# Optimization experiments

Measured on AMD Instinct MI355X. Metric: run time of the kernel, lower is better.

The kernel has to match this reference:

```python
import jax, jax.numpy as jnp
import numpy as np

K = 1024          # num_embeddings
D = 128           # embedding_dim
EMA_DECAY = 0.99
EPS = 1e-5


def setup_inputs() -> dict:
    key = jax.random.key(0)
    k1, k2, k3 = jax.random.split(key, 3)
    z = jax.random.normal(k1, (64, D, 32, 32), dtype=jnp.float32)
    codebook = jax.random.normal(k2, (K, D), dtype=jnp.float32)
    ema_count = jnp.zeros((K,), dtype=jnp.float32)
    ema_weight = jax.random.normal(k3, (K, D), dtype=jnp.float32)
    return {"z": z, "codebook": codebook, "ema_count": ema_count, "ema_weight": ema_weight}


def reference(z, codebook, ema_count, ema_weight):
    B, C, H, W = z.shape
    # flatten to [N, D] in BHWC order (matches permute(0,2,3,1).view(-1, D))
    z_flat = jnp.transpose(z, (0, 2, 3, 1)).reshape(-1, D)  # [N, D]

    # squared euclidean distances [N, K]
    distances = (
        jnp.sum(z_flat * z_flat, axis=1, keepdims=True)
        + jnp.sum(codebook * codebook, axis=1)
        - 2.0 * jnp.matmul(z_flat, codebook.T)
    )
    indices = jnp.argmin(distances, axis=1)  # [N] int

    # gather instead of one-hot @ codebook (same math)
    quantized_flat = codebook[indices]  # [N, D]
    # NOTE: faithful to original: raw view of BHWC-ordered flat buffer into z.shape
    quantized = quantized_flat.reshape(z.shape)

    # EMA statistics (no_grad in original): segment sums instead of one-hot matmuls
    encodings_sum = jax.ops.segment_sum(jnp.ones_like(indices, dtype=jnp.float32), indices, num_segments=K)
    dw = jax.ops.segment_sum(z_flat, indices, num_segments=K)  # [K, D]
    new_ema_count = EMA_DECAY * ema_count + (1.0 - EMA_DECAY) * encodings_sum
    new_ema_weight = EMA_DECAY * ema_weight + (1.0 - EMA_DECAY) * dw
    n = jnp.sum(new_ema_count)
    weights = (new_ema_count + EPS) / (n + K * EPS) * n
    new_codebook = new_ema_weight / weights[:, None]

    commitment_loss = jnp.mean((jax.lax.stop_gradient(quantized) - z) ** 2)
    codebook_loss = jnp.mean((quantized - jax.lax.stop_gradient(z)) ** 2)

    # straight-through estimator
    quantized_st = z + jax.lax.stop_gradient(quantized - z)

    idx_map = indices.reshape(B, H, W)
    return (quantized_st, idx_map, commitment_loss, codebook_loss,
            new_codebook, new_ema_count, new_ema_weight)
```

## Files before the change

### kernel.cpp

```cpp
#include <hip/hip_runtime.h>

#define NVEC 65536
#define KCB  1024
#define DIM  128
#define HW   1024
#define CHUNK 64
#define NCHUNKS (NVEC / CHUNK)

typedef __bf16 b16;
typedef b16 b16x8 __attribute__((ext_vector_type(8)));
typedef float f32x16 __attribute__((ext_vector_type(16)));

static __device__ __forceinline__ unsigned short f2bf(float f) {
  unsigned int x = __float_as_uint(f);
  unsigned int r = x + 0x7fffu + ((x >> 16) & 1u);
  return (unsigned short)(r >> 16);
}

__global__ void k_prep(const float* __restrict__ cb, const float* __restrict__ emw,
                       uint4* __restrict__ cbt, float* __restrict__ ccb,
                       double* __restrict__ cc64, float* __restrict__ out6,
                       int* __restrict__ hist) {
  const int t = blockIdx.x * blockDim.x + threadIdx.x;
  const int kc = t >> 11, u = t & 2047;
  const int code7 = u & 127, dch = u >> 7;
  const float* src = cb + (kc * 128 + code7) * 128 + dch * 8;
  const float4 x = *(const float4*)src;
  const float4 y = *(const float4*)(src + 4);
  uint4 o;
  o.x = (unsigned)f2bf(x.x) | ((unsigned)f2bf(x.y) << 16);
  o.y = (unsigned)f2bf(x.z) | ((unsigned)f2bf(x.w) << 16);
  o.z = (unsigned)f2bf(y.x) | ((unsigned)f2bf(y.y) << 16);
  o.w = (unsigned)f2bf(y.z) | ((unsigned)f2bf(y.w) << 16);
  cbt[t] = o;
  const float4 e0 = *(const float4*)(emw + (size_t)t * 8);
  const float4 e1 = *(const float4*)(emw + (size_t)t * 8 + 4);
  *(float2*)(out6 + (size_t)t * 8 + 0) = make_float2(0.99f * e0.x, 0.99f * e0.y);
  *(float2*)(out6 + (size_t)t * 8 + 2) = make_float2(0.99f * e0.z, 0.99f * e0.w);
  *(float2*)(out6 + (size_t)t * 8 + 4) = make_float2(0.99f * e1.x, 0.99f * e1.y);
  *(float2*)(out6 + (size_t)t * 8 + 6) = make_float2(0.99f * e1.z, 0.99f * e1.w);
  if (t < KCB) hist[t] = 0;
  if (blockIdx.x < 4) {
    const int k = blockIdx.x * 256 + threadIdx.x;
    const float* row = cb + k * DIM;
    double s = 0.0;
#pragma unroll 8
    for (int j = 0; j < DIM; ++j) {
      const double v = (double)row[j];
      s = fma(v, v, s);
    }
    cc64[k] = s;
    ccb[k] = 512.f - 0.5f * (float)s;
  }
}

__global__ __launch_bounds__(256, 4) void k_argmin3t(
    const float* __restrict__ z, const uint4* __restrict__ cbt,
    const float* __restrict__ ccb, uint2* __restrict__ pcand,
    float* __restrict__ z_t) {
  __shared__ __align__(16) char smem[128 * 65 * 4];
  float (*zs)[65] = (float(*)[65])smem;
  uint4* Bs = (uint4*)smem;
  const int tid = threadIdx.x;
  const int l = tid & 63, wv = tid >> 6;
  const int g = l >> 5;
  const int lm = l & 31;
  const int wr = (wv & 1) * 32;
  const int wc = wv >> 1;
  const int n0 = blockIdx.x * 64;
  const int b = n0 >> 10;
  const int hwbase = n0 & (HW - 1);

  {
    const int hw4 = (tid & 15) * 4;
    const int dr = tid >> 4;
    const float* src = z + (size_t)b * 131072 + hwbase + hw4;
#pragma unroll
    for (int j = 0; j < 8; ++j) {
      const int d = dr + 16 * j;
      const float4 v = *(const float4*)(src + d * 1024);
      zs[d][hw4 + 0] = v.x; zs[d][hw4 + 1] = v.y;
      zs[d][hw4 + 2] = v.z; zs[d][hw4 + 3] = v.w;
    }
  }
  __syncthreads();

#pragma unroll
  for (int jj = 0; jj < 2; ++jj) {
    const int row = (tid >> 3) + 32 * jj;
    float* dst = z_t + ((size_t)(n0 + row)) * 128;
#pragma unroll
    for (int j = 0; j < 4; ++j) {
      const int d = (j * 8 + (tid & 7)) * 4;
      float4 v;
      v.x = zs[d + 0][row]; v.y = zs[d + 1][row];
      v.z = zs[d + 2][row]; v.w = zs[d + 3][row];
      *(float4*)(dst + d) = v;
    }
  }
  uint4 afrag[8];
  {
    const int row = wr + lm;
#pragma unroll
    for (int ks = 0; ks < 8; ++ks) {
      const int d0 = ks * 16 + g * 8;
      afrag[ks].x = (unsigned)f2bf(zs[d0 + 0][row]) | ((unsigned)f2bf(zs[d0 + 1][row]) << 16);
      afrag[ks].y = (unsigned)f2bf(zs[d0 + 2][row]) | ((unsigned)f2bf(zs[d0 + 3][row]) << 16);
      afrag[ks].z = (unsigned)f2bf(zs[d0 + 4][row]) | ((unsigned)f2bf(zs[d0 + 5][row]) << 16);
      afrag[ks].w = (unsigned)f2bf(zs[d0 + 6][row]) | ((unsigned)f2bf(zs[d0 + 7][row]) << 16);
    }
  }

  unsigned pm1[16], pm2[16];
#pragma unroll
  for (int r = 0; r < 16; ++r) { pm1[r] = 0u; pm2[r] = 0u; }

  for (int kc = 0; kc < 8; ++kc) {
    __syncthreads();
#pragma unroll
    for (int i = 0; i < 8; ++i) {
      __builtin_amdgcn_global_load_lds(&cbt[kc * 2048 + wv * 512 + i * 64 + l],
                                       &Bs[wv * 512 + i * 64], 16, 0, 0);
    }
    const float cv0 = ccb[kc * 128 + (wc * 2 + 0) * 32 + lm];
    const float cv1 = ccb[kc * 128 + (wc * 2 + 1) * 32 + lm];
    __syncthreads();

    f32x16 a0, a1;
#pragma unroll
    for (int j = 0; j < 16; ++j) { a0[j] = cv0; a1[j] = cv1; }
#pragma unroll
    for (int ks = 0; ks < 8; ++ks) {
      const b16x8 av = *reinterpret_cast<const b16x8*>(&afrag[ks]);
      const b16x8 bv0 = *reinterpret_cast<const b16x8*>(&Bs[(ks * 2 + g) * 128 + (wc * 2) * 32 + lm]);
      const b16x8 bv1 = *reinterpret_cast<const b16x8*>(&Bs[(ks * 2 + g) * 128 + (wc * 2 + 1) * 32 + lm]);
      a0 = __builtin_amdgcn_mfma_f32_32x32x16_bf16(av, bv0, a0, 0, 0, 0);
      a1 = __builtin_amdgcn_mfma_f32_32x32x16_bf16(av, bv1, a1, 0, 0, 0);
    }
    const unsigned ci0 = 1023u - (unsigned)(kc * 128 + (wc * 2) * 32 + lm);
    const unsigned ci1 = ci0 - 32u;
#pragma unroll
    for (int r = 0; r < 16; ++r) {
      {
        const unsigned uu = ((__float_as_uint(a0[r]) + 0x200u) & 0xFFFFFC00u) | ci0;
        const unsigned t = pm1[r] < uu ? pm1[r] : uu;
        pm1[r] = pm1[r] > uu ? pm1[r] : uu;
        pm2[r] = pm2[r] > t ? pm2[r] : t;
      }
      {
        const unsigned uu = ((__float_as_uint(a1[r]) + 0x200u) & 0xFFFFFC00u) | ci1;
        const unsigned t = pm1[r] < uu ? pm1[r] : uu;
        pm1[r] = pm1[r] > uu ? pm1[r] : uu;
        pm2[r] = pm2[r] > t ? pm2[r] : t;
      }
    }
  }

#pragma unroll
  for (int r = 0; r < 16; ++r) {
    unsigned u1 = pm1[r], u2 = pm2[r];
#pragma unroll
    for (int m = 1; m < 32; m <<= 1) {
      const unsigned o1 = (unsigned)__shfl_xor((int)u1, m, 64);
      const unsigned o2 = (unsigned)__shfl_xor((int)u2, m, 64);
      const unsigned s = u1 < o1 ? u1 : o1;
      u1 = u1 > o1 ? u1 : o1;
      u2 = u2 > o2 ? u2 : o2;
      u2 = u2 > s ? u2 : s;
    }
    if (lm == 0) {
      const int rowg = n0 + wr + (r & 3) + 8 * (r >> 2) + 4 * g;
      pcand[wc * NVEC + rowg] = make_uint2(u1, u2);
    }
  }
}

__global__ void k_rescore_hist(const float* __restrict__ z_t, const float* __restrict__ cb,
                               const double* __restrict__ cc64,
                               const uint2* __restrict__ pcand,
                               float* __restrict__ out1, int* __restrict__ hist) {
  __shared__ int h[KCB];
  const int tid = threadIdx.x;
#pragma unroll
  for (int j = 0; j < 4; ++j) h[tid + 256 * j] = 0;
  __syncthreads();
  const int n = blockIdx.x * 256 + tid;
  const uint2 A = pcand[n];
  const uint2 Bq = pcand[NVEC + n];
  int ks[4];
  ks[0] = 1023 - (int)(A.x & 1023u);
  ks[1] = 1023 - (int)(A.y & 1023u);
  ks[2] = 1023 - (int)(Bq.x & 1023u);
  ks[3] = 1023 - (int)(Bq.y & 1023u);
  const float4* zr = (const float4*)(z_t + (size_t)n * DIM);
  const float4* c0 = (const float4*)(cb + ks[0] * DIM);
  const float4* c1 = (const float4*)(cb + ks[1] * DIM);
  const float4* c2 = (const float4*)(cb + ks[2] * DIM);
  const float4* c3 = (const float4*)(cb + ks[3] * DIM);
  double d0 = 0.0, d1 = 0.0, d2 = 0.0, d3 = 0.0;
#pragma unroll 4
  for (int j = 0; j < DIM / 4; ++j) {
    const float4 zv = zr[j];
    const double zx = zv.x, zy = zv.y, zz = zv.z, zw = zv.w;
    const float4 a = c0[j];
    d0 = fma(zx, (double)a.x, d0); d0 = fma(zy, (double)a.y, d0);
    d0 = fma(zz, (double)a.z, d0); d0 = fma(zw, (double)a.w, d0);
    const float4 b = c1[j];
    d1 = fma(zx, (double)b.x, d1); d1 = fma(zy, (double)b.y, d1);
    d1 = fma(zz, (double)b.z, d1); d1 = fma(zw, (double)b.w, d1);
    const float4 c = c2[j];
    d2 = fma(zx, (double)c.x, d2); d2 = fma(zy, (double)c.y, d2);
    d2 = fma(zz, (double)c.z, d2); d2 = fma(zw, (double)c.w, d2);
    const float4 e = c3[j];
    d3 = fma(zx, (double)e.x, d3); d3 = fma(zy, (double)e.y, d3);
    d3 = fma(zz, (double)e.z, d3); d3 = fma(zw, (double)e.w, d3);
  }
  double s[4];
  s[0] = fma(-2.0, d0, cc64[ks[0]]);
  s[1] = fma(-2.0, d1, cc64[ks[1]]);
  s[2] = fma(-2.0, d2, cc64[ks[2]]);
  s[3] = fma(-2.0, d3, cc64[ks[3]]);
  int kw = ks[0]; double sw = s[0];
#pragma unroll
  for (int c = 1; c < 4; ++c) {
    if (s[c] < sw || (s[c] == sw && ks[c] < kw)) { sw = s[c]; kw = ks[c]; }
  }
  out1[n] = (float)kw;
  atomicAdd(&h[kw], 1);
  __syncthreads();
#pragma unroll
  for (int j = 0; j < 4; ++j) {
    const int v = h[tid + 256 * j];
    if (v) atomicAdd(&hist[tid + 256 * j], v);
  }
}

__global__ void k_scan(const int* __restrict__ hist, const float* __restrict__ emc,
                       int* __restrict__ cursor, float* __restrict__ out5,
                       float* __restrict__ ntot) {
  __shared__ int tmp[KCB];
  __shared__ float red[16];
  const int t = threadIdx.x;
  const int v = hist[t];
  tmp[t] = v;
  __syncthreads();
  for (int off = 1; off < KCB; off <<= 1) {
    int x = 0;
    if (t >= off) x = tmp[t - off];
    __syncthreads();
    if (t >= off) tmp[t] += x;
    __syncthreads();
  }
  cursor[t] = tmp[t] - v;
  float o5 = 0.99f * emc[t] + 0.01f * (float)v;
  out5[t] = o5;
#pragma unroll
  for (int m = 32; m; m >>= 1) o5 += __shfl_xor(o5, m, 64);
  if ((t & 63) == 0) red[t >> 6] = o5;
  __syncthreads();
  if (t == 0) {
    float s = 0.f;
#pragma unroll
    for (int j = 0; j < 16; ++j) s += red[j];
    *ntot = s;
  }
}

__global__ void k_scatter(const float* __restrict__ idx_f, int* __restrict__ cursor,
                          int* __restrict__ order, int* __restrict__ key) {
  const int n = blockIdx.x * blockDim.x + threadIdx.x;
  const int k = (int)idx_f[n];
  const int pos = atomicAdd(&cursor[k], 1);
  order[pos] = n;
  key[pos] = k;
}

__global__ __launch_bounds__(128) void k_chunkreduce_q(
    float* zq, const float* __restrict__ cb,
    const int* __restrict__ order, const int* __restrict__ key,
    float* __restrict__ out6, float* __restrict__ lossp) {
  __shared__ int so[CHUNK], sk[CHUNK];
  __shared__ float red[2];
  const int t = threadIdx.x;
  const int base = blockIdx.x * CHUNK;
  if (t < CHUNK) { so[t] = order[base + t]; sk[t] = key[base + t]; }
  __syncthreads();
  int kprev = sk[0];
  float cbv = cb[kprev * 128 + t];
  float acc = 0.f, loss = 0.f;
  int i = 0;
  while (i < CHUNK) {
    if (i + 8 <= CHUNK && sk[i] == kprev && sk[i + 7] == kprev) {
      const int n0 = so[i + 0], n1 = so[i + 1], n2 = so[i + 2], n3 = so[i + 3];
      const int n4 = so[i + 4], n5 = so[i + 5], n6 = so[i + 6], n7 = so[i + 7];
      const float v0 = zq[(size_t)n0 * 128 + t];
      const float v1 = zq[(size_t)n1 * 128 + t];
      const float v2 = zq[(size_t)n2 * 128 + t];
      const float v3 = zq[(size_t)n3 * 128 + t];
      const float v4 = zq[(size_t)n4 * 128 + t];
      const float v5 = zq[(size_t)n5 * 128 + t];
      const float v6 = zq[(size_t)n6 * 128 + t];
      const float v7 = zq[(size_t)n7 * 128 + t];
      acc += ((v0 + v1) + (v2 + v3)) + ((v4 + v5) + (v6 + v7));
      float e;
      e = cbv - v0; loss = fmaf(e, e, loss);
      e = cbv - v1; loss = fmaf(e, e, loss);
      e = cbv - v2; loss = fmaf(e, e, loss);
      e = cbv - v3; loss = fmaf(e, e, loss);
      e = cbv - v4; loss = fmaf(e, e, loss);
      e = cbv - v5; loss = fmaf(e, e, loss);
      e = cbv - v6; loss = fmaf(e, e, loss);
      e = cbv - v7; loss = fmaf(e, e, loss);
      zq[(size_t)n0 * 128 + t] = cbv; zq[(size_t)n1 * 128 + t] = cbv;
      zq[(size_t)n2 * 128 + t] = cbv; zq[(size_t)n3 * 128 + t] = cbv;
      zq[(size_t)n4 * 128 + t] = cbv; zq[(size_t)n5 * 128 + t] = cbv;
      zq[(size_t)n6 * 128 + t] = cbv; zq[(size_t)n7 * 128 + t] = cbv;
      i += 8;
    } else {
      const int kk = sk[i];
      if (kk != kprev) {
        atomicAdd(&out6[kprev * 128 + t], 0.01f * acc);
        acc = 0.f; kprev = kk;
        cbv = cb[kk * 128 + t];
      }
      const int n = so[i];
      const float v = zq[(size_t)n * 128 + t];
      acc += v;
      const float e = cbv - v; loss = fmaf(e, e, loss);
      zq[(size_t)n * 128 + t] = cbv;
      ++i;
    }
  }
  atomicAdd(&out6[kprev * 128 + t], 0.01f * acc);
#pragma unroll
  for (int m = 32; m; m >>= 1) loss += __shfl_xor(loss, m, 64);
  if ((t & 63) == 0) red[t >> 6] = loss;
  __syncthreads();
  if (t == 0) lossp[blockIdx.x] = red[0] + red[1];
}

__global__ void k_final(const float* __restrict__ out5, const float* __restrict__ out6,
                        const float* __restrict__ ntot_p, const float* __restrict__ lossp,
                        float* __restrict__ out4, float* __restrict__ out2,
                        float* __restrict__ out3) {
  __shared__ float red[4];
  const int i = blockIdx.x * blockDim.x + threadIdx.x;
  const float ntot = *ntot_p;
  const int k = i >> 7;
  const float w = (out5[k] + 1e-5f) / (ntot + KCB * 1e-5f) * ntot;
  out4[i] = out6[i] / w;
  if (blockIdx.x == 511) {
    const int t = threadIdx.x;
    float s = 0.f;
#pragma unroll
    for (int j = 0; j < NCHUNKS / 256; ++j) s += lossp[t + 256 * j];
#pragma unroll
    for (int m = 32; m; m >>= 1) s += __shfl_xor(s, m, 64);
    if ((t & 63) == 0) red[t >> 6] = s;
    __syncthreads();
    if (t == 0) {
      const float lv = (red[0] + red[1] + red[2] + red[3]) * (1.f / 8388608.f);
      *out2 = lv; *out3 = lv;
    }
  }
}

extern "C" void kernel_launch(void* const* d_in, const int* in_sizes, int n_in,
                              void* d_out, int out_size, void* d_ws, size_t ws_size,
                              hipStream_t stream) {
  (void)in_sizes; (void)n_in; (void)out_size; (void)ws_size;
  const float* z   = (const float*)d_in[0];
  const float* cb  = (const float*)d_in[1];
  const float* emc = (const float*)d_in[2];
  const float* emw = (const float*)d_in[3];
  float* out = (float*)d_out;
  float* out0 = out;
  float* out1 = out + 8388608;
  float* out2 = out + 8454144;
  float* out3 = out + 8454145;
  float* out4 = out + 8454146;
  float* out5 = out + 8585218;
  float* out6 = out + 8586242;
  float* ws = (float*)d_ws;
  uint4* cbt      = (uint4*)ws;
  uint2* pcand    = (uint2*)(ws + 65536);
  int* order      = (int*)(ws + 65536);
  int* key        = (int*)(ws + 131072);
  float* ccb      = ws + 327680;
  int* hist       = (int*)(ws + 328704);
  int* cursor     = (int*)(ws + 329728);
  float* ntot     = ws + 330752;
  float* lossp    = ws + 331776;
  double* cc64    = (double*)(ws + 333824);
  float* z_t = out0;

  hipLaunchKernelGGL(k_prep, dim3(64), dim3(256), 0, stream, cb, emw, cbt, ccb,
                     cc64, out6, hist);
  hipLaunchKernelGGL(k_argmin3t, dim3(NVEC / 64), dim3(256), 0, stream,
                     z, cbt, ccb, pcand, z_t);
  hipLaunchKernelGGL(k_rescore_hist, dim3(NVEC / 256), dim3(256), 0, stream,
                     z_t, cb, cc64, pcand, out1, hist);
  hipLaunchKernelGGL(k_scan, dim3(1), dim3(1024), 0, stream, hist, emc, cursor,
                     out5, ntot);
  hipLaunchKernelGGL(k_scatter, dim3(NVEC / 256), dim3(256), 0, stream, out1, cursor,
                     order, key);
  hipLaunchKernelGGL(k_chunkreduce_q, dim3(NCHUNKS), dim3(128), 0, stream,
                     z_t, cb, order, key, out6, lossp);
  hipLaunchKernelGGL(k_final, dim3(512), dim3(256), 0, stream, out5, out6, ntot,
                     lossp, out4, out2, out3);
}
```

Baseline: 138.9 us.

## Fuse fp64 candidate rescoring and histogram into the argmin kernel

```diff
diff --git a/kernel.cpp b/kernel.cpp
--- a/kernel.cpp
+++ b/kernel.cpp
@@ -54,13 +54,14 @@
   }
 }
 
-__global__ __launch_bounds__(256, 4) void k_argmin3t(
+__global__ __launch_bounds__(256, 4) void k_argmin6(
     const float* __restrict__ z, const uint4* __restrict__ cbt,
-    const float* __restrict__ ccb, uint2* __restrict__ pcand,
-    float* __restrict__ z_t) {
-  __shared__ __align__(16) char smem[128 * 65 * 4];
-  float (*zs)[65] = (float(*)[65])smem;
-  uint4* Bs = (uint4*)smem;
+    const float* __restrict__ ccb, const double* __restrict__ cc64,
+    const float* __restrict__ cb, float* __restrict__ z_t,
+    float* __restrict__ out1, int* __restrict__ hist) {
+  __shared__ __align__(16) float zs[128][65];
+  __shared__ uint2 cand[64][2];
+  uint4* Bs = (uint4*)zs;
   const int tid = threadIdx.x;
   const int l = tid & 63, wv = tid >> 6;
   const int g = l >> 5;
@@ -169,64 +170,45 @@
       u2 = u2 > s ? u2 : s;
     }
     if (lm == 0) {
-      const int rowg = n0 + wr + (r & 3) + 8 * (r >> 2) + 4 * g;
-      pcand[wc * NVEC + rowg] = make_uint2(u1, u2);
-    }
-  }
-}
-
-__global__ void k_rescore_hist(const float* __restrict__ z_t, const float* __restrict__ cb,
-                               const double* __restrict__ cc64,
-                               const uint2* __restrict__ pcand,
-                               float* __restrict__ out1, int* __restrict__ hist) {
-  __shared__ int h[KCB];
-  const int tid = threadIdx.x;
+      const int lrow = wr + (r & 3) + 8 * (r >> 2) + 4 * g;
+      cand[lrow][wc] = make_uint2(u1, u2);
+    }
+  }
+  __syncthreads();
+
+  int* h = (int*)zs;
 #pragma unroll
   for (int j = 0; j < 4; ++j) h[tid + 256 * j] = 0;
   __syncthreads();
-  const int n = blockIdx.x * 256 + tid;
-  const uint2 A = pcand[n];
-  const uint2 Bq = pcand[NVEC + n];
-  int ks[4];
-  ks[0] = 1023 - (int)(A.x & 1023u);
-  ks[1] = 1023 - (int)(A.y & 1023u);
-  ks[2] = 1023 - (int)(Bq.x & 1023u);
-  ks[3] = 1023 - (int)(Bq.y & 1023u);
-  const float4* zr = (const float4*)(z_t + (size_t)n * DIM);
-  const float4* c0 = (const float4*)(cb + ks[0] * DIM);
-  const float4* c1 = (const float4*)(cb + ks[1] * DIM);
-  const float4* c2 = (const float4*)(cb + ks[2] * DIM);
-  const float4* c3 = (const float4*)(cb + ks[3] * DIM);
-  double d0 = 0.0, d1 = 0.0, d2 = 0.0, d3 = 0.0;
-#pragma unroll 4
-  for (int j = 0; j < DIM / 4; ++j) {
-    const float4 zv = zr[j];
-    const double zx = zv.x, zy = zv.y, zz = zv.z, zw = zv.w;
-    const float4 a = c0[j];
-    d0 = fma(zx, (double)a.x, d0); d0 = fma(zy, (double)a.y, d0);
-    d0 = fma(zz, (double)a.z, d0); d0 = fma(zw, (double)a.w, d0);
-    const float4 b = c1[j];
-    d1 = fma(zx, (double)b.x, d1); d1 = fma(zy, (double)b.y, d1);
-    d1 = fma(zz, (double)b.z, d1); d1 = fma(zw, (double)b.w, d1);
-    const float4 c = c2[j];
-    d2 = fma(zx, (double)c.x, d2); d2 = fma(zy, (double)c.y, d2);
-    d2 = fma(zz, (double)c.z, d2); d2 = fma(zw, (double)c.w, d2);
-    const float4 e = c3[j];
-    d3 = fma(zx, (double)e.x, d3); d3 = fma(zy, (double)e.y, d3);
-    d3 = fma(zz, (double)e.z, d3); d3 = fma(zw, (double)e.w, d3);
-  }
-  double s[4];
-  s[0] = fma(-2.0, d0, cc64[ks[0]]);
-  s[1] = fma(-2.0, d1, cc64[ks[1]]);
-  s[2] = fma(-2.0, d2, cc64[ks[2]]);
-  s[3] = fma(-2.0, d3, cc64[ks[3]]);
-  int kw = ks[0]; double sw = s[0];
-#pragma unroll
-  for (int c = 1; c < 4; ++c) {
-    if (s[c] < sw || (s[c] == sw && ks[c] < kw)) { sw = s[c]; kw = ks[c]; }
-  }
-  out1[n] = (float)kw;
-  atomicAdd(&h[kw], 1);
+  {
+    const int row = tid >> 2, c = tid & 3;
+    const uint2 cd = cand[row][c >> 1];
+    const unsigned u = (c & 1) ? cd.y : cd.x;
+    int k = 1023 - (int)(u & 1023u);
+    const int n = n0 + row;
+    const float4* zr = (const float4*)(z_t + (size_t)n * DIM);
+    const float4* cr = (const float4*)(cb + k * DIM);
+    double d = 0.0;
+#pragma unroll 8
+    for (int j = 0; j < DIM / 4; ++j) {
+      const float4 zv = zr[j], cv = cr[j];
+      d = fma((double)zv.x, (double)cv.x, d);
+      d = fma((double)zv.y, (double)cv.y, d);
+      d = fma((double)zv.z, (double)cv.z, d);
+      d = fma((double)zv.w, (double)cv.w, d);
+    }
+    double s = fma(-2.0, d, cc64[k]);
+#pragma unroll
+    for (int m = 1; m < 4; m <<= 1) {
+      const double os = __shfl_xor(s, m, 64);
+      const int ok = __shfl_xor(k, m, 64);
+      if (os < s || (os == s && ok < k)) { s = os; k = ok; }
+    }
+    if (c == 0) {
+      out1[n] = (float)k;
+      atomicAdd(&h[k], 1);
+    }
+  }
   __syncthreads();
 #pragma unroll
   for (int j = 0; j < 4; ++j) {
@@ -383,7 +365,6 @@
   float* out6 = out + 8586242;
   float* ws = (float*)d_ws;
   uint4* cbt      = (uint4*)ws;
-  uint2* pcand    = (uint2*)(ws + 65536);
   int* order      = (int*)(ws + 65536);
   int* key        = (int*)(ws + 131072);
   float* ccb      = ws + 327680;
@@ -396,10 +377,8 @@
 
   hipLaunchKernelGGL(k_prep, dim3(64), dim3(256), 0, stream, cb, emw, cbt, ccb,
                      cc64, out6, hist);
-  hipLaunchKernelGGL(k_argmin3t, dim3(NVEC / 64), dim3(256), 0, stream,
-                     z, cbt, ccb, pcand, z_t);
-  hipLaunchKernelGGL(k_rescore_hist, dim3(NVEC / 256), dim3(256), 0, stream,
-                     z_t, cb, cc64, pcand, out1, hist);
+  hipLaunchKernelGGL(k_argmin6, dim3(NVEC / 64), dim3(256), 0, stream,
+                     z, cbt, ccb, cc64, cb, z_t, out1, hist);
   hipLaunchKernelGGL(k_scan, dim3(1), dim3(1024), 0, stream, hist, emc, cursor,
                      out5, ntot);
   hipLaunchKernelGGL(k_scatter, dim3(NVEC / 256), dim3(256), 0, stream, out1, cursor,
```

Result: faster. 129.8 us (-6.6%).
